# Optimization experiments

Hardware: AMD Instinct MI355X
Metric: run time of the kernel (lower is better)

## Reference

```python
import jax, jax.numpy as jnp
import numpy as np
from jax.ops import segment_sum, segment_max

N = 50000
E = 800000
IN_C, HID_C, OUT_C, HEADS = 64, 128, 32, 4
BN_EPS = 1e-5
NEG_SLOPE = 0.2


def setup_inputs() -> dict:
    key = jax.random.key(0)
    ks = jax.random.split(key, 16)
    s = 0.1  # weight scale for numerical sanity
    inp = {
        'x': jax.random.normal(ks[0], (N, IN_C), jnp.float32),
        'edge_index': jax.random.randint(ks[1], (2, E), 0, N, jnp.int64),
        'sage1_wl': jax.random.normal(ks[2], (IN_C, HID_C), jnp.float32) * s,
        'sage1_bl': jnp.zeros((HID_C,), jnp.float32),
        'sage1_wr': jax.random.normal(ks[3], (IN_C, HID_C), jnp.float32) * s,
        'bn1_gamma': jnp.ones((HID_C,), jnp.float32),
        'bn1_beta': jnp.zeros((HID_C,), jnp.float32),
        'bn1_mean': jnp.zeros((HID_C,), jnp.float32),
        'bn1_var': jnp.ones((HID_C,), jnp.float32),
        'sage2_wl': jax.random.normal(ks[4], (HID_C, HID_C), jnp.float32) * s,
        'sage2_bl': jnp.zeros((HID_C,), jnp.float32),
        'sage2_wr': jax.random.normal(ks[5], (HID_C, HID_C), jnp.float32) * s,
        'bn2_gamma': jnp.ones((HID_C,), jnp.float32),
        'bn2_beta': jnp.zeros((HID_C,), jnp.float32),
        'bn2_mean': jnp.zeros((HID_C,), jnp.float32),
        'bn2_var': jnp.ones((HID_C,), jnp.float32),
        'gat_w': jax.random.normal(ks[6], (HID_C, HEADS * OUT_C), jnp.float32) * s,
        'gat_att_src': jax.random.normal(ks[7], (HEADS, OUT_C), jnp.float32) * s,
        'gat_att_dst': jax.random.normal(ks[8], (HEADS, OUT_C), jnp.float32) * s,
        'gat_bias': jnp.zeros((OUT_C,), jnp.float32),
        'cls_w1': jax.random.normal(ks[9], (OUT_C, 64), jnp.float32) * s,
        'cls_b1': jnp.zeros((64,), jnp.float32),
        'cls_w2': jax.random.normal(ks[10], (64, 1), jnp.float32) * s,
        'cls_b2': jnp.zeros((1,), jnp.float32),
    }
    return inp


def _sage_conv(x, src, dst, n, wl, bl, wr):
    # PyG SAGEConv (mean aggr): lin_l(mean_{j in N(i)} x_j) + lin_r(x_i)
    agg = segment_sum(x[src], dst, num_segments=n)           # [N, C]
    cnt = segment_sum(jnp.ones((src.shape[0], 1), x.dtype), dst, num_segments=n)
    mean = agg / jnp.maximum(cnt, 1.0)
    return mean @ wl + bl + x @ wr


def _bn_eval(x, gamma, beta, mean, var):
    return (x - mean) * jax.lax.rsqrt(var + BN_EPS) * gamma + beta


def _gat_conv(x, src, dst, n, w, att_src, att_dst, bias):
    # PyG GATConv, concat=False (head-average), add_self_loops=True
    loop = jnp.arange(n, dtype=src.dtype)
    s = jnp.concatenate([src, loop])
    d = jnp.concatenate([dst, loop])
    h = (x @ w).reshape(n, HEADS, OUT_C)                     # [N, H, C]
    a_src = jnp.einsum('nhc,hc->nh', h, att_src)             # [N, H]
    a_dst = jnp.einsum('nhc,hc->nh', h, att_dst)             # [N, H]
    e = jax.nn.leaky_relu(a_src[s] + a_dst[d], NEG_SLOPE)    # [Etot, H]
    m = segment_max(e, d, num_segments=n)                    # stable softmax per dst
    ex = jnp.exp(e - m[d])
    den = segment_sum(ex, d, num_segments=n)
    alpha = ex / den[d]                                      # [Etot, H]
    out = segment_sum(alpha[:, :, None] * h[s], d, num_segments=n)  # [N, H, C]
    return out.mean(axis=1) + bias                           # concat=False -> mean over heads


def reference(x, edge_index,
              sage1_wl, sage1_bl, sage1_wr,
              bn1_gamma, bn1_beta, bn1_mean, bn1_var,
              sage2_wl, sage2_bl, sage2_wr,
              bn2_gamma, bn2_beta, bn2_mean, bn2_var,
              gat_w, gat_att_src, gat_att_dst, gat_bias,
              cls_w1, cls_b1, cls_w2, cls_b2):
    n = x.shape[0]
    src, dst = edge_index[0], edge_index[1]
    # Layer 0: SAGE(64->128) + BN + ReLU (no residual: shapes differ); dropout = eval noop
    h = _sage_conv(x, src, dst, n, sage1_wl, sage1_bl, sage1_wr)
    h = jax.nn.relu(_bn_eval(h, bn1_gamma, bn1_beta, bn1_mean, bn1_var))
    # Layer 1: SAGE(128->128) + BN + residual + ReLU
    identity = h
    h2 = _sage_conv(h, src, dst, n, sage2_wl, sage2_bl, sage2_wr)
    h2 = _bn_eval(h2, bn2_gamma, bn2_beta, bn2_mean, bn2_var) + identity
    h2 = jax.nn.relu(h2)
    # Final layer: GAT head (128 -> 32, 4 heads averaged)
    embeddings = _gat_conv(h2, src, dst, n, gat_w, gat_att_src, gat_att_dst, gat_bias)
    # MLP classifier (dropout eval noop)
    logits = jax.nn.relu(embeddings @ cls_w1 + cls_b1) @ cls_w2 + cls_b2
    return embeddings, logits
```

## Files before the change

### kernel.cpp

```cpp
#include <hip/hip_runtime.h>

typedef unsigned int uint_t;
typedef unsigned short ush;
typedef short bf16x8 __attribute__((ext_vector_type(8)));
typedef float f32x4 __attribute__((ext_vector_type(4)));

constexpr int TPB = 256;
#define LOG2E 1.4426950408889634f

__device__ __forceinline__ float lrelu(float x){ return fmaxf(x, 0.f) + 0.2f*fminf(x, 0.f); }
__device__ __forceinline__ ush f2b(float f){
  uint_t u = __float_as_uint(f);
  return (ush)((u + 0x7fffu + ((u >> 16) & 1u)) >> 16);
}
__device__ __forceinline__ float b2f(ush s){ return __uint_as_float(((uint_t)s) << 16); }
__device__ __forceinline__ float blo(uint_t u){ return __uint_as_float(u << 16); }
__device__ __forceinline__ float bhi(uint_t u){ return __uint_as_float(u & 0xffff0000u); }

__global__ void k_bnfold(const float* __restrict__ g1, const float* __restrict__ b1,
                         const float* __restrict__ m1, const float* __restrict__ v1,
                         const float* __restrict__ g2, const float* __restrict__ b2,
                         const float* __restrict__ m2, const float* __restrict__ v2,
                         float* __restrict__ out){
  int t = threadIdx.x;
  int o = t & 127;
  bool second = t >= 128;
  const float* g = second ? g2 : g1;  const float* b = second ? b2 : b1;
  const float* m = second ? m2 : m1;  const float* v = second ? v2 : v1;
  float sc = g[o] * rsqrtf(v[o] + 1e-5f);
  float sh = b[o] - m[o]*sc;
  int off = second ? 256 : 0;
  out[off + o] = sc;
  out[off + 128 + o] = sh;
}

__global__ void k_deg(const int* __restrict__ dst, int* __restrict__ degi, int E){
  int t = blockIdx.x*TPB + threadIdx.x;
  if (t < E) atomicAdd(&degi[dst[t]], 1);
}

__global__ __launch_bounds__(1024) void k_scan1(const int* __restrict__ deg,
                                                int* __restrict__ out,
                                                int* __restrict__ bsum, int n){
  __shared__ int ws[16];
  int tid = threadIdx.x;
  int gid = blockIdx.x*1024 + tid;
  int v = (gid < n) ? deg[gid] : 0;
  int lane = tid & 63, wid = tid >> 6;
  int s = v;
  for (int off = 1; off < 64; off <<= 1){
    int t2 = __shfl_up(s, off);
    if (lane >= off) s += t2;
  }
  if (lane == 63) ws[wid] = s;
  __syncthreads();
  if (wid == 0){
    int w = (lane < 16) ? ws[lane] : 0;
    for (int off = 1; off < 16; off <<= 1){
      int t2 = __shfl_up(w, off);
      if (lane >= off) w += t2;
    }
    if (lane < 16) ws[lane] = w;
  }
  __syncthreads();
  int base = wid > 0 ? ws[wid-1] : 0;
  int incl = base + s;
  if (gid < n) out[gid] = incl - v;
  if (tid == 1023) bsum[blockIdx.x] = incl;
}

__global__ void k_scan2(int* __restrict__ bsum, int nb){
  int lane = threadIdx.x;
  int carry = 0;
  for (int base = 0; base < nb; base += 64){
    int i = base + lane;
    int v = (i < nb) ? bsum[i] : 0;
    int s = v;
    for (int off = 1; off < 64; off <<= 1){
      int t2 = __shfl_up(s, off);
      if (lane >= off) s += t2;
    }
    if (i < nb) bsum[i] = carry + s - v;
    int tot = __shfl(s, 63);
    carry += tot;
  }
  if (lane == 0) bsum[nb] = carry;
}

__global__ void k_scan3(int* __restrict__ offs, const int* __restrict__ bsum, int n, int nb){
  int gid = blockIdx.x*TPB + threadIdx.x;
  if (gid < n) offs[gid] += bsum[gid >> 10];
  else if (gid == n) offs[n] = bsum[nb];
}

__global__ void k_fill(const int* __restrict__ src, const int* __restrict__ dst,
                       const int* __restrict__ offs, int* __restrict__ cur,
                       ush* __restrict__ esrc, int E){
  int t = blockIdx.x*TPB + threadIdx.x;
  if (t >= E) return;
  int d = dst[t];
  int p = offs[d] + atomicAdd(&cur[d], 1);
  esrc[p] = (ush)src[t];
}

__global__ void k_tobf16(const float* __restrict__ in, ush* __restrict__ out, int n4){
  int t = blockIdx.x*TPB + threadIdx.x;
  if (t >= n4) return;
  float4 v = *(const float4*)(in + (size_t)t*4);
  ushort4 o;
  o.x = f2b(v.x); o.y = f2b(v.y); o.z = f2b(v.z); o.w = f2b(v.w);
  *(ushort4*)(out + (size_t)t*4) = o;
}

__global__ void k_wprep(const float* __restrict__ wr, const float* __restrict__ wl,
                        int C1, int K, ush* __restrict__ WT){
  int t = blockIdx.x*TPB + threadIdx.x;
  if (t >= 128*K) return;
  int n = t / K, k = t % K;
  float v = (k < C1) ? wr[(size_t)k*128 + n] : wl[(size_t)(k - C1)*128 + n];
  WT[t] = f2b(v);
}

template<int C>
__global__ __launch_bounds__(256) void k_gather_mean_b(
    const int* __restrict__ offs, const ush* __restrict__ esrc,
    const uint_t* __restrict__ xb, uint_t* __restrict__ meanb, int n){
  constexpr int L = C/2;
  int tid = threadIdx.x;
  int nid = blockIdx.x*(256/L) + tid/L;
  uint_t l = tid % L;
  if (nid >= n) return;
  int k0 = offs[nid], k1 = offs[nid+1];
  const ush* sp = esrc + k0;
  int cnt = k1 - k0;
  float s0 = 0.f, s1 = 0.f;
  int k = 0;
  for (; k + 8 <= cnt; k += 8){
    uint_t e0 = sp[k],   e1 = sp[k+1], e2 = sp[k+2], e3 = sp[k+3];
    uint_t e4 = sp[k+4], e5 = sp[k+5], e6 = sp[k+6], e7 = sp[k+7];
    uint_t u0 = xb[e0*L + l];
    uint_t u1 = xb[e1*L + l];
    uint_t u2 = xb[e2*L + l];
    uint_t u3 = xb[e3*L + l];
    uint_t u4 = xb[e4*L + l];
    uint_t u5 = xb[e5*L + l];
    uint_t u6 = xb[e6*L + l];
    uint_t u7 = xb[e7*L + l];
    s0 += ((blo(u0) + blo(u1)) + (blo(u2) + blo(u3)))
        + ((blo(u4) + blo(u5)) + (blo(u6) + blo(u7)));
    s1 += ((bhi(u0) + bhi(u1)) + (bhi(u2) + bhi(u3)))
        + ((bhi(u4) + bhi(u5)) + (bhi(u6) + bhi(u7)));
  }
  for (; k + 4 <= cnt; k += 4){
    uint_t e0 = sp[k], e1 = sp[k+1], e2 = sp[k+2], e3 = sp[k+3];
    uint_t u0 = xb[e0*L + l];
    uint_t u1 = xb[e1*L + l];
    uint_t u2 = xb[e2*L + l];
    uint_t u3 = xb[e3*L + l];
    s0 += (blo(u0) + blo(u1)) + (blo(u2) + blo(u3));
    s1 += (bhi(u0) + bhi(u1)) + (bhi(u2) + bhi(u3));
  }
  for (; k < cnt; ++k){
    uint_t u = xb[(uint_t)sp[k]*L + l];
    s0 += blo(u);
    s1 += bhi(u);
  }
  float inv = 1.f / (float)max(cnt, 1);
  uint_t lo = f2b(s0*inv), hi = f2b(s1*inv);
  meanb[(uint_t)nid*L + l] = lo | (hi << 16);
}

template<int K, bool BN, bool RES_LDS, bool RELU, bool ATTN>
__global__ __launch_bounds__(256) void k_mm_mfma(
    const ush* __restrict__ A1, int C1,
    const ush* __restrict__ A2,
    const ush* __restrict__ WT,
    const float* __restrict__ bias,
    const float* __restrict__ bnp, int bnoff,
    const float* __restrict__ atts, const float* __restrict__ attd,
    float* __restrict__ asrc_o, float* __restrict__ adst_o,
    ush* __restrict__ outb, int n)
{
  constexpr int PAD = K + 8;
  __shared__ ush sA[32][PAD];
  int tid = threadIdx.x;
  int wave = tid >> 6, lane = tid & 63;
  int node0 = blockIdx.x * 32;
  int C2 = K - C1;

  for (int idx = tid; idx < 32*(K/8); idx += 256) {
    int r  = idx / (K/8);
    int kc = (idx % (K/8)) * 8;
    int g = node0 + r;
    uint4 v = make_uint4(0,0,0,0);
    if (g < n) {
      if (kc < C1) v = *(const uint4*)(A1 + (size_t)g*C1 + kc);
      else         v = *(const uint4*)(A2 + (size_t)g*C2 + (kc - C1));
    }
    *(uint4*)&sA[r][kc] = v;
  }
  __syncthreads();

  f32x4 acc[2][2] = {};
  int l15 = lane & 15, lk = (lane >> 4) * 8;
  const ush* wt0 = WT + (size_t)(wave*32 + l15) * K + lk;
  const ush* wt1 = wt0 + (size_t)16 * K;

  #pragma unroll
  for (int kk = 0; kk < K; kk += 32) {
    bf16x8 a0 = *(const bf16x8*)&sA[l15][kk + lk];
    bf16x8 a1 = *(const bf16x8*)&sA[16 + l15][kk + lk];
    bf16x8 b0 = *(const bf16x8*)(wt0 + kk);
    bf16x8 b1 = *(const bf16x8*)(wt1 + kk);
    acc[0][0] = __builtin_amdgcn_mfma_f32_16x16x32_bf16(a0, b0, acc[0][0], 0, 0, 0);
    acc[0][1] = __builtin_amdgcn_mfma_f32_16x16x32_bf16(a0, b1, acc[0][1], 0, 0, 0);
    acc[1][0] = __builtin_amdgcn_mfma_f32_16x16x32_bf16(a1, b0, acc[1][0], 0, 0, 0);
    acc[1][1] = __builtin_amdgcn_mfma_f32_16x16x32_bf16(a1, b1, acc[1][1], 0, 0, 0);
  }

  int r0 = (lane >> 4) * 4;
  #pragma unroll
  for (int mt = 0; mt < 2; ++mt) {
    #pragma unroll
    for (int nt = 0; nt < 2; ++nt) {
      int nn = wave*32 + nt*16 + l15;
      float bv = bias ? bias[nn] : 0.f;
      float sc = 1.f, sh = 0.f;
      if constexpr (BN) { sc = bnp[bnoff + nn]; sh = bnp[bnoff + 128 + nn]; }
      #pragma unroll
      for (int j = 0; j < 4; ++j) {
        int r = mt*16 + r0 + j;
        int g = node0 + r;
        if (g < n) {
          float v = acc[mt][nt][j] + bv;
          if constexpr (BN)      v = v*sc + sh;
          if constexpr (RES_LDS) v += b2f(sA[r][nn]);
          if constexpr (RELU)    v = fmaxf(v, 0.f);
          outb[(size_t)g*128 + nn] = f2b(v);
        }
      }
    }
  }

  if constexpr (ATTN) {
    float as0 = atts[wave*32 + l15],      ad0 = attd[wave*32 + l15];
    float as1 = atts[wave*32 + 16 + l15], ad1 = attd[wave*32 + 16 + l15];
    #pragma unroll
    for (int mt = 0; mt < 2; ++mt) {
      #pragma unroll
      for (int j = 0; j < 4; ++j) {
        float v0 = acc[mt][0][j], v1 = acc[mt][1][j];
        float ps = fmaf(v0, as0, v1 * as1);
        float pd = fmaf(v0, ad0, v1 * ad1);
        ps += __shfl_xor(ps, 1); ps += __shfl_xor(ps, 2);
        ps += __shfl_xor(ps, 4); ps += __shfl_xor(ps, 8);
        pd += __shfl_xor(pd, 1); pd += __shfl_xor(pd, 2);
        pd += __shfl_xor(pd, 4); pd += __shfl_xor(pd, 8);
        int g = node0 + mt*16 + r0 + j;
        if (l15 == 0 && g < n) {
          asrc_o[(uint_t)g*4 + wave] = ps * LOG2E;
          adst_o[(uint_t)g*4 + wave] = pd * LOG2E;
        }
      }
    }
  }
}

__global__ __launch_bounds__(256) void k_gat(
    const int* __restrict__ offs, const ush* __restrict__ esrc,
    const float* __restrict__ asrc, const float* __restrict__ adst,
    const uint_t* __restrict__ hgb, const float* __restrict__ gbias,
    const float* __restrict__ w1, const float* __restrict__ b1,
    const float* __restrict__ w2, const float* __restrict__ b2,
    float* __restrict__ out_emb, float* __restrict__ out_log, int n){
  __shared__ float semb[4][32];
  int tid = threadIdx.x;
  int wl = tid >> 6;
  uint_t l = tid & 63;
  int nid = blockIdx.x*4 + wl;
  if (nid >= n) return;
  uint_t h = l >> 4;
  uint_t i4 = (uint_t)nid*4 + h;
  float ad = adst[i4];
  float e0 = exp2f(lrelu(asrc[i4] + ad));
  uint_t u = hgb[(uint_t)nid*64 + l];
  float accD  = e0;
  float accN0 = e0 * blo(u);
  float accN1 = e0 * bhi(u);
  int k0 = offs[nid], k1 = offs[nid+1];
  const ush* sp = esrc + k0;
  int cnt = k1 - k0;
  int k = 0;
  for (; k + 8 <= cnt; k += 8){
    uint_t s0 = sp[k],   s1 = sp[k+1], s2 = sp[k+2], s3 = sp[k+3];
    uint_t s4 = sp[k+4], s5 = sp[k+5], s6 = sp[k+6], s7 = sp[k+7];
    float a0 = asrc[s0*4 + h], a1 = asrc[s1*4 + h];
    float a2 = asrc[s2*4 + h], a3 = asrc[s3*4 + h];
    float a4 = asrc[s4*4 + h], a5 = asrc[s5*4 + h];
    float a6 = asrc[s6*4 + h], a7 = asrc[s7*4 + h];
    uint_t v0 = hgb[s0*64 + l];
    uint_t v1 = hgb[s1*64 + l];
    uint_t v2 = hgb[s2*64 + l];
    uint_t v3 = hgb[s3*64 + l];
    uint_t v4 = hgb[s4*64 + l];
    uint_t v5 = hgb[s5*64 + l];
    uint_t v6 = hgb[s6*64 + l];
    uint_t v7 = hgb[s7*64 + l];
    float e0_ = exp2f(lrelu(a0 + ad));
    float e1_ = exp2f(lrelu(a1 + ad));
    float e2_ = exp2f(lrelu(a2 + ad));
    float e3_ = exp2f(lrelu(a3 + ad));
    float e4_ = exp2f(lrelu(a4 + ad));
    float e5_ = exp2f(lrelu(a5 + ad));
    float e6_ = exp2f(lrelu(a6 + ad));
    float e7_ = exp2f(lrelu(a7 + ad));
    accD += ((e0_ + e1_) + (e2_ + e3_)) + ((e4_ + e5_) + (e6_ + e7_));
    accN0 = fmaf(e0_, blo(v0), accN0);
    accN0 = fmaf(e1_, blo(v1), accN0);
    accN0 = fmaf(e2_, blo(v2), accN0);
    accN0 = fmaf(e3_, blo(v3), accN0);
    accN0 = fmaf(e4_, blo(v4), accN0);
    accN0 = fmaf(e5_, blo(v5), accN0);
    accN0 = fmaf(e6_, blo(v6), accN0);
    accN0 = fmaf(e7_, blo(v7), accN0);
    accN1 = fmaf(e0_, bhi(v0), accN1);
    accN1 = fmaf(e1_, bhi(v1), accN1);
    accN1 = fmaf(e2_, bhi(v2), accN1);
    accN1 = fmaf(e3_, bhi(v3), accN1);
    accN1 = fmaf(e4_, bhi(v4), accN1);
    accN1 = fmaf(e5_, bhi(v5), accN1);
    accN1 = fmaf(e6_, bhi(v6), accN1);
    accN1 = fmaf(e7_, bhi(v7), accN1);
  }
  if (k + 4 <= cnt){
    uint_t s0 = sp[k], s1 = sp[k+1], s2 = sp[k+2], s3 = sp[k+3];
    float a0 = asrc[s0*4 + h], a1 = asrc[s1*4 + h];
    float a2 = asrc[s2*4 + h], a3 = asrc[s3*4 + h];
    uint_t v0 = hgb[s0*64 + l];
    uint_t v1 = hgb[s1*64 + l];
    uint_t v2 = hgb[s2*64 + l];
    uint_t v3 = hgb[s3*64 + l];
    float e0_ = exp2f(lrelu(a0 + ad));
    float e1_ = exp2f(lrelu(a1 + ad));
    float e2_ = exp2f(lrelu(a2 + ad));
    float e3_ = exp2f(lrelu(a3 + ad));
    accD += (e0_ + e1_) + (e2_ + e3_);
    accN0 = fmaf(e0_, blo(v0), accN0);
    accN0 = fmaf(e1_, blo(v1), accN0);
    accN0 = fmaf(e2_, blo(v2), accN0);
    accN0 = fmaf(e3_, blo(v3), accN0);
    accN1 = fmaf(e0_, bhi(v0), accN1);
    accN1 = fmaf(e1_, bhi(v1), accN1);
    accN1 = fmaf(e2_, bhi(v2), accN1);
    accN1 = fmaf(e3_, bhi(v3), accN1);
    k += 4;
  }
  for (; k < cnt; ++k){
    uint_t s = sp[k];
    float e = exp2f(lrelu(asrc[s*4 + h] + ad));
    uint_t v = hgb[s*64 + l];
    accD += e;
    accN0 = fmaf(e, blo(v), accN0);
    accN1 = fmaf(e, bhi(v), accN1);
  }
  float inv = 1.f / accD;
  float v0 = accN0 * inv, v1 = accN1 * inv;
  v0 += __shfl_xor(v0, 16); v0 += __shfl_xor(v0, 32);
  v1 += __shfl_xor(v1, 16); v1 += __shfl_xor(v1, 32);
  if (l < 16){
    int c = l*2;
    float2 o;
    o.x = 0.25f*v0 + gbias[c];
    o.y = 0.25f*v1 + gbias[c+1];
    *(float2*)(out_emb + (size_t)nid*32 + c) = o;
    semb[wl][c] = o.x;
    semb[wl][c+1] = o.y;
  }
  float a = b1[l];
  #pragma unroll
  for (int c = 0; c < 32; ++c) a = fmaf(semb[wl][c], w1[c*64 + l], a);
  float t = fmaxf(a, 0.f) * w2[l];
  t += __shfl_xor(t, 1);  t += __shfl_xor(t, 2);  t += __shfl_xor(t, 4);
  t += __shfl_xor(t, 8);  t += __shfl_xor(t, 16); t += __shfl_xor(t, 32);
  if (l == 0) out_log[nid] = t + b2[0];
}

extern "C" void kernel_launch(void* const* d_in, const int* in_sizes, int n_in,
                              void* d_out, int out_size, void* d_ws, size_t ws_size,
                              hipStream_t stream) {
  const float* x    = (const float*)d_in[0];
  const int*   ei   = (const int*)  d_in[1];
  const float* s1wl = (const float*)d_in[2];
  const float* s1bl = (const float*)d_in[3];
  const float* s1wr = (const float*)d_in[4];
  const float* bn1g = (const float*)d_in[5];
  const float* bn1b = (const float*)d_in[6];
  const float* bn1m = (const float*)d_in[7];
  const float* bn1v = (const float*)d_in[8];
  const float* s2wl = (const float*)d_in[9];
  const float* s2bl = (const float*)d_in[10];
  const float* s2wr = (const float*)d_in[11];
  const float* bn2g = (const float*)d_in[12];
  const float* bn2b = (const float*)d_in[13];
  const float* bn2m = (const float*)d_in[14];
  const float* bn2v = (const float*)d_in[15];
  const float* gatw = (const float*)d_in[16];
  const float* atts = (const float*)d_in[17];
  const float* attd = (const float*)d_in[18];
  const float* gatb = (const float*)d_in[19];
  const float* cw1  = (const float*)d_in[20];
  const float* cb1  = (const float*)d_in[21];
  const float* cw2  = (const float*)d_in[22];
  const float* cb2  = (const float*)d_in[23];

  const int N = in_sizes[0] / 64;
  const int E = in_sizes[1] / 2;
  const int* src = ei;
  const int* dst = ei + E;
  const int NBK = (N + 1023) / 1024;

  float* asrc = (float*)d_ws;
  float* adst = asrc + (size_t)N*4;
  float* bnp  = adst + (size_t)N*4;
  ush* regA = (ush*)(bnp + 512);
  ush* regB = regA + (size_t)N*128;
  ush* regC = regB + (size_t)N*128;
  ush* W1T  = regC + (size_t)N*128;
  ush* W2T  = W1T + 128*128;
  ush* WGT  = W2T + 128*256;
  int* degi = (int*)(WGT + 128*128);
  int* offs = degi + N;
  int* cur  = offs + N + 1;
  ush* esrc = (ush*)(cur + N);
  int* bsum = (int*)(esrc + E + (E & 1));

  ush* xb     = regA;
  ush* mean1b = regA + (size_t)N*64;
  ush* mean2b = regA;
  ush* h1b    = regB;
  ush* hgb    = regB;
  ush* h2b    = regC;

  float* out_emb = (float*)d_out;
  float* out_log = out_emb + (size_t)N*32;

  hipMemsetAsync(degi, 0, (size_t)N*4, stream);
  hipMemsetAsync(cur,  0, (size_t)N*4, stream);

  k_bnfold<<<1, 256, 0, stream>>>(bn1g,bn1b,bn1m,bn1v, bn2g,bn2b,bn2m,bn2v, bnp);

  k_deg<<<(E+TPB-1)/TPB, TPB, 0, stream>>>(dst, degi, E);
  k_scan1<<<NBK, 1024, 0, stream>>>(degi, offs, bsum, N);
  k_scan2<<<1, 64, 0, stream>>>(bsum, NBK);
  k_scan3<<<(N+1+TPB-1)/TPB, TPB, 0, stream>>>(offs, bsum, N, NBK);
  k_fill<<<(E+TPB-1)/TPB, TPB, 0, stream>>>(src, dst, offs, cur, esrc, E);

  k_wprep<<<(128*128+TPB-1)/TPB, TPB, 0, stream>>>(s1wr, s1wl, 64, 128, W1T);
  k_wprep<<<(128*256+TPB-1)/TPB, TPB, 0, stream>>>(s2wr, s2wl, 128, 256, W2T);
  k_wprep<<<(128*128+TPB-1)/TPB, TPB, 0, stream>>>(gatw, nullptr, 128, 128, WGT);

  k_tobf16<<<(N*16+TPB-1)/TPB, TPB, 0, stream>>>(x, xb, N*16);

  int nmm = (N + 31) / 32;

  k_gather_mean_b<64><<<(N+7)/8, 256, 0, stream>>>(offs, esrc, (const uint_t*)xb, (uint_t*)mean1b, N);
  k_mm_mfma<128,true,false,true,false><<<nmm, 256, 0, stream>>>(
      xb, 64, mean1b, W1T, s1bl, bnp, 0, nullptr, nullptr, nullptr, nullptr, h1b, N);

  k_gather_mean_b<128><<<(N+3)/4, 256, 0, stream>>>(offs, esrc, (const uint_t*)h1b, (uint_t*)mean2b, N);
  k_mm_mfma<256,true,true,true,false><<<nmm, 256, 0, stream>>>(
      h1b, 128, mean2b, W2T, s2bl, bnp, 256, nullptr, nullptr, nullptr, nullptr, h2b, N);

  k_mm_mfma<128,false,false,false,true><<<nmm, 256, 0, stream>>>(
      h2b, 128, nullptr, WGT, nullptr, bnp, 0, atts, attd, asrc, adst, hgb, N);

  k_gat<<<(N+3)/4, 256, 0, stream>>>(offs, esrc, asrc, adst, (const uint_t*)hgb, gatb,
                                     cw1, cb1, cw2, cb2, out_emb, out_log, N);
}
```

Before: 257.1 us.

## Fuse neighbor mean gather into SAGE MFMA matmul kernels via LDS

Removes the separate gather-mean kernels and computes each node's neighbor mean directly into the shared-memory A tile of the MFMA matmul, so the mean never takes a round trip through global memory and two launches go away. Edge source indices are now read as packed 32-bit pairs in both the gather and the GAT kernel, with a peel step for odd offsets. The cost is that each matmul block does its own serialized gather (8 nodes per wave, 4-wide unroll instead of 8), which may lower memory-level parallelism and occupancy for the latency-bound gather.

Result: slower. 267.4 us (+4.0%).

```diff
diff --git a/kernel.cpp b/kernel.cpp
--- a/kernel.cpp
+++ b/kernel.cpp
@@ -121,59 +121,10 @@
   WT[t] = f2b(v);
 }
 
-template<int C>
-__global__ __launch_bounds__(256) void k_gather_mean_b(
+template<int K, int C1, bool BN, bool RES_LDS, bool RELU, bool ATTN, bool GATHER>
+__global__ __launch_bounds__(256) void k_mm_mfma(
+    const ush* __restrict__ table,
     const int* __restrict__ offs, const ush* __restrict__ esrc,
-    const uint_t* __restrict__ xb, uint_t* __restrict__ meanb, int n){
-  constexpr int L = C/2;
-  int tid = threadIdx.x;
-  int nid = blockIdx.x*(256/L) + tid/L;
-  uint_t l = tid % L;
-  if (nid >= n) return;
-  int k0 = offs[nid], k1 = offs[nid+1];
-  const ush* sp = esrc + k0;
-  int cnt = k1 - k0;
-  float s0 = 0.f, s1 = 0.f;
-  int k = 0;
-  for (; k + 8 <= cnt; k += 8){
-    uint_t e0 = sp[k],   e1 = sp[k+1], e2 = sp[k+2], e3 = sp[k+3];
-    uint_t e4 = sp[k+4], e5 = sp[k+5], e6 = sp[k+6], e7 = sp[k+7];
-    uint_t u0 = xb[e0*L + l];
-    uint_t u1 = xb[e1*L + l];
-    uint_t u2 = xb[e2*L + l];
-    uint_t u3 = xb[e3*L + l];
-    uint_t u4 = xb[e4*L + l];
-    uint_t u5 = xb[e5*L + l];
-    uint_t u6 = xb[e6*L + l];
-    uint_t u7 = xb[e7*L + l];
-    s0 += ((blo(u0) + blo(u1)) + (blo(u2) + blo(u3)))
-        + ((blo(u4) + blo(u5)) + (blo(u6) + blo(u7)));
-    s1 += ((bhi(u0) + bhi(u1)) + (bhi(u2) + bhi(u3)))
-        + ((bhi(u4) + bhi(u5)) + (bhi(u6) + bhi(u7)));
-  }
-  for (; k + 4 <= cnt; k += 4){
-    uint_t e0 = sp[k], e1 = sp[k+1], e2 = sp[k+2], e3 = sp[k+3];
-    uint_t u0 = xb[e0*L + l];
-    uint_t u1 = xb[e1*L + l];
-    uint_t u2 = xb[e2*L + l];
-    uint_t u3 = xb[e3*L + l];
-    s0 += (blo(u0) + blo(u1)) + (blo(u2) + blo(u3));
-    s1 += (bhi(u0) + bhi(u1)) + (bhi(u2) + bhi(u3));
-  }
-  for (; k < cnt; ++k){
-    uint_t u = xb[(uint_t)sp[k]*L + l];
-    s0 += blo(u);
-    s1 += bhi(u);
-  }
-  float inv = 1.f / (float)max(cnt, 1);
-  uint_t lo = f2b(s0*inv), hi = f2b(s1*inv);
-  meanb[(uint_t)nid*L + l] = lo | (hi << 16);
-}
-
-template<int K, bool BN, bool RES_LDS, bool RELU, bool ATTN>
-__global__ __launch_bounds__(256) void k_mm_mfma(
-    const ush* __restrict__ A1, int C1,
-    const ush* __restrict__ A2,
     const ush* __restrict__ WT,
     const float* __restrict__ bias,
     const float* __restrict__ bnp, int bnoff,
@@ -186,18 +137,57 @@
   int tid = threadIdx.x;
   int wave = tid >> 6, lane = tid & 63;
   int node0 = blockIdx.x * 32;
-  int C2 = K - C1;
-
-  for (int idx = tid; idx < 32*(K/8); idx += 256) {
-    int r  = idx / (K/8);
-    int kc = (idx % (K/8)) * 8;
+
+  for (int idx = tid; idx < 32*(C1/8); idx += 256) {
+    int r  = idx / (C1/8);
+    int kc = (idx % (C1/8)) * 8;
     int g = node0 + r;
     uint4 v = make_uint4(0,0,0,0);
-    if (g < n) {
-      if (kc < C1) v = *(const uint4*)(A1 + (size_t)g*C1 + kc);
-      else         v = *(const uint4*)(A2 + (size_t)g*C2 + (kc - C1));
+    if (g < n) v = *(const uint4*)(table + (size_t)g*C1 + kc);
+    *(uint4*)&sA[r][kc] = v;
+  }
+
+  if constexpr (GATHER) {
+    const uint_t* t32 = (const uint_t*)table;
+    constexpr int L2u = (K - C1) / 2;
+    constexpr int NPI = 64 / L2u;
+    for (int i = 0; i < 8; i += NPI) {
+      int r = wave*8 + i + (NPI == 2 ? (lane >> 5) : 0);
+      uint_t l = (NPI == 2) ? (lane & 31) : lane;
+      int g = node0 + r;
+      float s0 = 0.f, s1 = 0.f;
+      int cnt = 0;
+      if (g < n) {
+        int kk0 = offs[g], kk1 = offs[g+1];
+        cnt = kk1 - kk0;
+        const ush* sp = esrc + kk0;
+        int k = 0;
+        if ((kk0 & 1) && cnt > 0) {
+          uint_t u = t32[(uint_t)sp[0]*L2u + l];
+          s0 += blo(u); s1 += bhi(u);
+          k = 1;
+        }
+        const uint_t* sp2 = (const uint_t*)(sp + k);
+        for (; k + 4 <= cnt; k += 4) {
+          uint_t pa = sp2[0], pb = sp2[1]; sp2 += 2;
+          uint_t e0 = pa & 0xffffu, e1 = pa >> 16;
+          uint_t e2 = pb & 0xffffu, e3 = pb >> 16;
+          uint_t u0 = t32[e0*L2u + l];
+          uint_t u1 = t32[e1*L2u + l];
+          uint_t u2 = t32[e2*L2u + l];
+          uint_t u3 = t32[e3*L2u + l];
+          s0 += (blo(u0) + blo(u1)) + (blo(u2) + blo(u3));
+          s1 += (bhi(u0) + bhi(u1)) + (bhi(u2) + bhi(u3));
+        }
+        for (; k < cnt; ++k) {
+          uint_t u = t32[(uint_t)sp[k]*L2u + l];
+          s0 += blo(u); s1 += bhi(u);
+        }
+      }
+      float inv = 1.f / (float)max(cnt, 1);
+      uint_t lo = f2b(s0*inv), hi = f2b(s1*inv);
+      ((uint_t*)&sA[r][C1])[l] = lo | (hi << 16);
     }
-    *(uint4*)&sA[r][kc] = v;
   }
   __syncthreads();
 
@@ -291,9 +281,22 @@
   const ush* sp = esrc + k0;
   int cnt = k1 - k0;
   int k = 0;
+  if ((k0 & 1) && cnt > 0){
+    uint_t s = sp[0];
+    float e = exp2f(lrelu(asrc[s*4 + h] + ad));
+    uint_t v = hgb[s*64 + l];
+    accD += e;
+    accN0 = fmaf(e, blo(v), accN0);
+    accN1 = fmaf(e, bhi(v), accN1);
+    k = 1;
+  }
+  const uint_t* sp2 = (const uint_t*)(sp + k);
   for (; k + 8 <= cnt; k += 8){
-    uint_t s0 = sp[k],   s1 = sp[k+1], s2 = sp[k+2], s3 = sp[k+3];
-    uint_t s4 = sp[k+4], s5 = sp[k+5], s6 = sp[k+6], s7 = sp[k+7];
+    uint_t p0 = sp2[0], p1 = sp2[1], p2 = sp2[2], p3 = sp2[3]; sp2 += 4;
+    uint_t s0 = p0 & 0xffffu, s1 = p0 >> 16;
+    uint_t s2 = p1 & 0xffffu, s3 = p1 >> 16;
+    uint_t s4 = p2 & 0xffffu, s5 = p2 >> 16;
+    uint_t s6 = p3 & 0xffffu, s7 = p3 >> 16;
     float a0 = asrc[s0*4 + h], a1 = asrc[s1*4 + h];
     float a2 = asrc[s2*4 + h], a3 = asrc[s3*4 + h];
     float a4 = asrc[s4*4 + h], a5 = asrc[s5*4 + h];
@@ -333,7 +336,9 @@
     accN1 = fmaf(e7_, bhi(v7), accN1);
   }
   if (k + 4 <= cnt){
-    uint_t s0 = sp[k], s1 = sp[k+1], s2 = sp[k+2], s3 = sp[k+3];
+    uint_t p0 = sp2[0], p1 = sp2[1]; sp2 += 2;
+    uint_t s0 = p0 & 0xffffu, s1 = p0 >> 16;
+    uint_t s2 = p1 & 0xffffu, s3 = p1 >> 16;
     float a0 = asrc[s0*4 + h], a1 = asrc[s1*4 + h];
     float a2 = asrc[s2*4 + h], a3 = asrc[s3*4 + h];
     uint_t v0 = hgb[s0*64 + l];
@@ -423,7 +428,7 @@
   float* adst = asrc + (size_t)N*4;
   float* bnp  = adst + (size_t)N*4;
   ush* regA = (ush*)(bnp + 512);
-  ush* regB = regA + (size_t)N*128;
+  ush* regB = regA + (size_t)N*64;
   ush* regC = regB + (size_t)N*128;
   ush* W1T  = regC + (size_t)N*128;
   ush* W2T  = W1T + 128*128;
@@ -434,12 +439,10 @@
   ush* esrc = (ush*)(cur + N);
   int* bsum = (int*)(esrc + E + (E & 1));
 
-  ush* xb     = regA;
-  ush* mean1b = regA + (size_t)N*64;
-  ush* mean2b = regA;
-  ush* h1b    = regB;
-  ush* hgb    = regB;
-  ush* h2b    = regC;
+  ush* xb  = regA;
+  ush* h1b = regB;
+  ush* hgb = regB;
+  ush* h2b = regC;
 
   float* out_emb = (float*)d_out;
   float* out_log = out_emb + (size_t)N*32;
@@ -463,16 +466,14 @@
 
   int nmm = (N + 31) / 32;
 
-  k_gather_mean_b<64><<<(N+7)/8, 256, 0, stream>>>(offs, esrc, (const uint_t*)xb, (uint_t*)mean1b, N);
-  k_mm_mfma<128,true,false,true,false><<<nmm, 256, 0, stream>>>(
-      xb, 64, mean1b, W1T, s1bl, bnp, 0, nullptr, nullptr, nullptr, nullptr, h1b, N);
-
-  k_gather_mean_b<128><<<(N+3)/4, 256, 0, stream>>>(offs, esrc, (const uint_t*)h1b, (uint_t*)mean2b, N);
-  k_mm_mfma<256,true,true,true,false><<<nmm, 256, 0, stream>>>(
-      h1b, 128, mean2b, W2T, s2bl, bnp, 256, nullptr, nullptr, nullptr, nullptr, h2b, N);
-
-  k_mm_mfma<128,false,false,false,true><<<nmm, 256, 0, stream>>>(
-      h2b, 128, nullptr, WGT, nullptr, bnp, 0, atts, attd, asrc, adst, hgb, N);
+  k_mm_mfma<128,64,true,false,true,false,true><<<nmm, 256, 0, stream>>>(
+      xb, offs, esrc, W1T, s1bl, bnp, 0, nullptr, nullptr, nullptr, nullptr, h1b, N);
+
+  k_mm_mfma<256,128,true,true,true,false,true><<<nmm, 256, 0, stream>>>(
+      h1b, offs, esrc, W2T, s2bl, bnp, 256, nullptr, nullptr, nullptr, nullptr, h2b, N);
+
+  k_mm_mfma<128,128,false,false,false,true,false><<<nmm, 256, 0, stream>>>(
+      h2b, nullptr, nullptr, WGT, nullptr, bnp, 0, atts, attd, asrc, adst, hgb, N);
 
   k_gat<<<(N+3)/4, 256, 0, stream>>>(offs, esrc, asrc, adst, (const uint_t*)hgb, gatb,
                                      cw1, cb1, cw2, cb2, out_emb, out_log, N);
```
